# Kernel optimization log

Measured on AMD Instinct MI355X. Metric: run time of the kernel, lower is better.

Reference implementation:

```python
import jax, jax.numpy as jnp
import numpy as np

N = 100000      # nodes
E = 3200000     # edges
G = 256         # graphs in batch
EPS = 1e-5      # BatchNorm eps


def gcn_conv(x, W, b, src, dst, norm):
    # x: [N, Fin] -> [N, Fout]. PyG GCNConv: linear, then sym-normalized
    # scatter-add over edges (self-loops already included in src/dst/norm).
    h = x @ W                                   # [N, Fout]
    msg = h[src] * norm[:, None]                # [E+N, Fout] gather + scale
    out = jax.ops.segment_sum(msg, dst, num_segments=N)
    return out + b


def bn_eval(x, gamma, beta, rm, rv):
    return (x - rm) * jax.lax.rsqrt(rv + EPS) * gamma + beta


def setup_inputs() -> dict:
    key = jax.random.key(0)
    ks = jax.random.split(key, 24)
    x = jax.random.normal(ks[0], (N, 8), dtype=jnp.float32)
    edge_index = jax.random.randint(ks[1], (2, E), 0, N, dtype=jnp.int64)
    batch = jnp.sort(jax.random.randint(ks[2], (N,), 0, G, dtype=jnp.int64))

    def lin(k, fin, fout):
        return jax.random.normal(k, (fin, fout), dtype=jnp.float32) / np.sqrt(fin)

    d = {
        "x": x, "edge_index": edge_index, "batch": batch,
        "W1": lin(ks[3], 8, 64),  "b1": jnp.zeros((64,), jnp.float32),
        "g1": jnp.ones((64,), jnp.float32), "be1": jnp.zeros((64,), jnp.float32),
        "rm1": jax.random.normal(ks[4], (64,), jnp.float32) * 0.1,
        "rv1": jnp.ones((64,), jnp.float32) + jax.random.uniform(ks[5], (64,)) * 0.1,
        "W2": lin(ks[6], 64, 64), "b2": jnp.zeros((64,), jnp.float32),
        "g2": jnp.ones((64,), jnp.float32), "be2": jnp.zeros((64,), jnp.float32),
        "rm2": jax.random.normal(ks[7], (64,), jnp.float32) * 0.1,
        "rv2": jnp.ones((64,), jnp.float32) + jax.random.uniform(ks[8], (64,)) * 0.1,
        "W3": lin(ks[9], 64, 64), "b3": jnp.zeros((64,), jnp.float32),
        "g3": jnp.ones((64,), jnp.float32), "be3": jnp.zeros((64,), jnp.float32),
        "rm3": jax.random.normal(ks[10], (64,), jnp.float32) * 0.1,
        "rv3": jnp.ones((64,), jnp.float32) + jax.random.uniform(ks[11], (64,)) * 0.1,
        "Wr1": lin(ks[12], 64, 64), "br1": jnp.zeros((64,), jnp.float32),
        "Wr2": lin(ks[13], 64, 2),  "br2": jnp.zeros((2,), jnp.float32),
    }
    return d


def reference(x, edge_index, batch,
              W1, b1, g1, be1, rm1, rv1,
              W2, b2, g2, be2, rm2, rv2,
              W3, b3, g3, be3, rm3, rv3,
              Wr1, br1, Wr2, br2):
    # add self-loops once; compute symmetric normalization deg^-1/2
    loops = jnp.arange(N, dtype=edge_index.dtype)
    src = jnp.concatenate([edge_index[0], loops])   # [E+N]
    dst = jnp.concatenate([edge_index[1], loops])
    deg = jax.ops.segment_sum(jnp.ones_like(dst, dtype=x.dtype), dst, num_segments=N)
    dinv = jnp.where(deg > 0, jax.lax.rsqrt(deg), 0.0)
    norm = dinv[src] * dinv[dst]                    # [E+N]

    h = jax.nn.relu(bn_eval(gcn_conv(x, W1, b1, src, dst, norm), g1, be1, rm1, rv1))
    h = jax.nn.relu(bn_eval(gcn_conv(h, W2, b2, src, dst, norm), g2, be2, rm2, rv2))
    h = jax.nn.relu(bn_eval(gcn_conv(h, W3, b3, src, dst, norm), g3, be3, rm3, rv3))

    # global mean pool over graph ids
    sums = jax.ops.segment_sum(h, batch, num_segments=G)           # [G, 64]
    cnts = jax.ops.segment_sum(jnp.ones((N,), h.dtype), batch, num_segments=G)
    pooled = sums / jnp.maximum(cnts, 1.0)[:, None]

    out = jax.nn.relu(pooled @ Wr1 + br1) @ Wr2 + br2              # [G, 2]
    return out
```

## Files before the change

### kernel.cpp

```cpp
#include <hip/hip_runtime.h>

#define NN 100000
#define NE 3200000
#define NG 256
#define NF (NN * 64)
#define FEPS 1e-5f
#define BSH 8
#define NB ((NN + 255) >> 8)
#define CHA 8192

static inline int ceil_div(int a, int b) { return (a + b - 1) / b; }


__global__ __launch_bounds__(256) void kA_hist(const int* __restrict__ dst,
                                               int* __restrict__ bh) {
    __shared__ int lh[NB];
    int t = threadIdx.x;
    for (int b = t; b < NB; b += 256) lh[b] = 0;
    __syncthreads();
    int e0 = blockIdx.x * CHA;
    int e1 = min(e0 + CHA, NE);
    for (int i = e0 + t; i < e1; i += 256) atomicAdd(&lh[dst[i] >> BSH], 1);
    __syncthreads();
    for (int b = t; b < NB; b += 256)
        if (lh[b]) atomicAdd(&bh[b], lh[b]);
}

__global__ __launch_bounds__(512) void kA_scan(const int* __restrict__ bh,
                                               int* __restrict__ bboff,
                                               int* __restrict__ bcur) {
    __shared__ int s[512];
    int t = threadIdx.x;
    int v = (t < NB) ? bh[t] : 0;
    s[t] = v;
    __syncthreads();
    for (int off = 1; off < 512; off <<= 1) {
        int add = (t >= off) ? s[t - off] : 0;
        __syncthreads();
        s[t] += add;
        __syncthreads();
    }
    if (t < NB) {
        int ex = s[t] - v;
        bboff[t] = ex;
        bcur[t] = ex;
    }
    if (t == 0) bboff[NB] = NE;
}

__global__ __launch_bounds__(256) void kA_fill(const int* __restrict__ src,
                                               const int* __restrict__ dst,
                                               int* __restrict__ bcur,
                                               int2* __restrict__ ebuf) {
    __shared__ int lh[NB];
    __shared__ int lbase[NB];
    __shared__ int lcur[NB];
    int t = threadIdx.x;
    for (int b = t; b < NB; b += 256) lh[b] = 0;
    __syncthreads();
    int e0 = blockIdx.x * CHA;
    int e1 = min(e0 + CHA, NE);
    for (int i = e0 + t; i < e1; i += 256) atomicAdd(&lh[dst[i] >> BSH], 1);
    __syncthreads();
    for (int b = t; b < NB; b += 256) {
        int c = lh[b];
        lbase[b] = c ? atomicAdd(&bcur[b], c) : 0;
        lcur[b] = 0;
    }
    __syncthreads();
    for (int i = e0 + t; i < e1; i += 256) {
        int d = dst[i];
        int s = src[i];
        int b = d >> BSH;
        int p = atomicAdd(&lcur[b], 1);
        ebuf[lbase[b] + p] = make_int2(s, d);
    }
}


__global__ __launch_bounds__(256) void kB_hist(const int2* __restrict__ ebuf,
                                               const int* __restrict__ bboff,
                                               int* __restrict__ cnt) {
    __shared__ int lc[256];
    int b = blockIdx.x;
    int t = threadIdx.x;
    lc[t] = 0;
    __syncthreads();
    int st = bboff[b], en = bboff[b + 1];
    for (int i = st + t; i < en; i += 256) atomicAdd(&lc[ebuf[i].y & 255], 1);
    __syncthreads();
    int node = (b << BSH) + t;
    if (node < NN) cnt[node] = lc[t];
}

__global__ __launch_bounds__(256) void k_dinv_xs(const int* __restrict__ cnt,
                                                 const float* __restrict__ x,
                                                 float* __restrict__ dinv,
                                                 float* __restrict__ xs) {
    int i = blockIdx.x * 256 + threadIdx.x;
    if (i >= NN) return;
    float di = rsqrtf((float)cnt[i] + 1.0f);
    dinv[i] = di;
#pragma unroll
    for (int f = 0; f < 8; ++f) xs[i * 8 + f] = x[i * 8 + f] * di;
}

__global__ __launch_bounds__(256) void k_scan1(const int* __restrict__ cnt,
                                               int* __restrict__ bsum) {
    __shared__ int s[256];
    int t = threadIdx.x;
    int i = blockIdx.x * 256 + t;
    s[t] = (i < NN) ? cnt[i] : 0;
    __syncthreads();
    for (int off = 128; off > 0; off >>= 1) {
        if (t < off) s[t] += s[t + off];
        __syncthreads();
    }
    if (t == 0) bsum[blockIdx.x] = s[0];
}

__global__ __launch_bounds__(512) void k_scan2(int* __restrict__ bsum, int nb) {
    __shared__ int s[512];
    int t = threadIdx.x;
    int v = (t < nb) ? bsum[t] : 0;
    s[t] = v;
    __syncthreads();
    for (int off = 1; off < 512; off <<= 1) {
        int add = (t >= off) ? s[t - off] : 0;
        __syncthreads();
        s[t] += add;
        __syncthreads();
    }
    if (t < nb) bsum[t] = s[t] - v;
}

__global__ __launch_bounds__(256) void k_scan3(const int* __restrict__ cnt,
                                               const int* __restrict__ bsum,
                                               int* __restrict__ rowptr) {
    __shared__ int s[256];
    int t = threadIdx.x;
    int i = blockIdx.x * 256 + t;
    int v = (i < NN) ? cnt[i] : 0;
    s[t] = v;
    __syncthreads();
    for (int off = 1; off < 256; off <<= 1) {
        int add = (t >= off) ? s[t - off] : 0;
        __syncthreads();
        s[t] += add;
        __syncthreads();
    }
    if (i < NN) rowptr[i] = s[t] - v + bsum[blockIdx.x];
}

__global__ __launch_bounds__(256) void kB_fill(const int2* __restrict__ ebuf,
                                               const int* __restrict__ bboff,
                                               const int* __restrict__ rowptr,
                                               int* __restrict__ csr) {
    __shared__ int rp[256];
    __shared__ int lc[256];
    int b = blockIdx.x;
    int t = threadIdx.x;
    int node = (b << BSH) + t;
    rp[t] = (node < NN) ? rowptr[node] : 0;
    lc[t] = 0;
    __syncthreads();
    int st = bboff[b], en = bboff[b + 1];
    for (int i = st + t; i < en; i += 256) {
        int2 e = ebuf[i];
        int dl = e.y & 255;
        int p = atomicAdd(&lc[dl], 1);
        csr[rp[dl] + p] = e.x;
    }
}


__global__ __launch_bounds__(256) void k_gxf8(const float* __restrict__ xs,
                                              const int* __restrict__ rowptr,
                                              const int* __restrict__ cnt,
                                              const float* __restrict__ dinv,
                                              const int* __restrict__ csr,
                                              const float* __restrict__ W,
                                              const float* __restrict__ b,
                                              const float* __restrict__ g,
                                              const float* __restrict__ be,
                                              const float* __restrict__ rm,
                                              const float* __restrict__ rv,
                                              float* __restrict__ out) {
    __shared__ float Ws[512];
    int tid = threadIdx.x;
    for (int i = tid; i < 512; i += 256) Ws[i] = W[i];
    __syncthreads();
    int wave = (blockIdx.x * 256 + tid) >> 6;
    int lane = tid & 63;
    if (wave >= NN) return;
    int es = lane >> 3, f = lane & 7;
    int st = rowptr[wave], n = cnt[wave];
    float acc = 0.f;
    for (int k0 = 0; k0 < n; k0 += 8) {
        int kk = k0 + es;
        if (kk < n) acc += xs[csr[st + kk] * 8 + f];
    }
    acc += __shfl_xor(acc, 8, 64);
    acc += __shfl_xor(acc, 16, 64);
    acc += __shfl_xor(acc, 32, 64);
    float di = dinv[wave];
    float pf = (acc + xs[wave * 8 + f]) * di;
    float scale = g[lane] * rsqrtf(rv[lane] + FEPS);
    float shift = be[lane] + (b[lane] - rm[lane]) * scale;
    float o = 0.f;
#pragma unroll
    for (int k = 0; k < 8; ++k)
        o = fmaf(__shfl(pf, k, 64), Ws[k * 64 + lane], o);
    o = fmaxf(fmaf(o, scale, shift), 0.f);
    out[wave * 64 + lane] = o * di;
}

template <bool SCALE_OUT>
__global__ __launch_bounds__(256) void k_gxf64(const float* __restrict__ Hin,
                                               const int* __restrict__ rowptr,
                                               const int* __restrict__ cnt,
                                               const float* __restrict__ dinv,
                                               const int* __restrict__ csr,
                                               const float* __restrict__ W,
                                               const float* __restrict__ b,
                                               const float* __restrict__ g,
                                               const float* __restrict__ be,
                                               const float* __restrict__ rm,
                                               const float* __restrict__ rv,
                                               float* __restrict__ out) {
    __shared__ float Ws[4096];
    int tid = threadIdx.x;
    for (int i = tid; i < 4096; i += 256) Ws[i] = W[i];
    __syncthreads();
    int wave = (blockIdx.x * 256 + tid) >> 6;
    int lane = tid & 63;
    if (wave >= NN) return;
    int st = rowptr[wave], n = cnt[wave];
    float acc = Hin[wave * 64 + lane];
    int k = 0;
    for (; k + 4 <= n; k += 4) {
        int s0 = csr[st + k];
        int s1 = csr[st + k + 1];
        int s2 = csr[st + k + 2];
        int s3 = csr[st + k + 3];
        float v0 = Hin[s0 * 64 + lane];
        float v1 = Hin[s1 * 64 + lane];
        float v2 = Hin[s2 * 64 + lane];
        float v3 = Hin[s3 * 64 + lane];
        acc += v0; acc += v1; acc += v2; acc += v3;
    }
    for (; k < n; ++k) acc += Hin[csr[st + k] * 64 + lane];
    float di = dinv[wave];
    float pf = acc * di;
    float scale = g[lane] * rsqrtf(rv[lane] + FEPS);
    float shift = be[lane] + (b[lane] - rm[lane]) * scale;
    float o = 0.f;
#pragma unroll
    for (int k2 = 0; k2 < 64; ++k2)
        o = fmaf(__shfl(pf, k2, 64), Ws[k2 * 64 + lane], o);
    o = fmaxf(fmaf(o, scale, shift), 0.f);
    if (SCALE_OUT) o *= di;
    out[wave * 64 + lane] = o;
}


__global__ __launch_bounds__(256) void k_pool(const float* __restrict__ h,
                                              const int* __restrict__ batch,
                                              float* __restrict__ sums,
                                              float* __restrict__ cnts) {
    const int CHUNK = 32;
    int gw = (blockIdx.x * 256 + threadIdx.x) >> 6;
    int lane = threadIdx.x & 63;
    int nw = (gridDim.x * 256) >> 6;
    int nchunks = (NN + CHUNK - 1) / CHUNK;
    for (int c = gw; c < nchunks; c += nw) {
        int n0 = c * CHUNK;
        int n1 = min(n0 + CHUNK, NN);
        int gcur = batch[n0];
        float accf = 0.f;
        float cntf = 0.f;
        for (int n = n0; n < n1; ++n) {
            int gg = batch[n];
            if (gg != gcur) {
                atomicAdd(&sums[gcur * 64 + lane], accf);
                if (lane == 0) atomicAdd(&cnts[gcur], cntf);
                accf = 0.f;
                cntf = 0.f;
                gcur = gg;
            }
            accf += h[n * 64 + lane];
            cntf += 1.f;
        }
        atomicAdd(&sums[gcur * 64 + lane], accf);
        if (lane == 0) atomicAdd(&cnts[gcur], cntf);
    }
}

__global__ __launch_bounds__(256) void k_head(const float* __restrict__ sums,
                                              const float* __restrict__ cnts,
                                              const float* __restrict__ Wr1,
                                              const float* __restrict__ br1,
                                              const float* __restrict__ Wr2,
                                              const float* __restrict__ br2,
                                              float* __restrict__ out) {
    int wave = (blockIdx.x * 256 + threadIdx.x) >> 6;
    int lane = threadIdx.x & 63;
    if (wave >= NG) return;
    float c = fmaxf(cnts[wave], 1.0f);
    float pooled = sums[wave * 64 + lane] / c;
    float acc = 0.f;
#pragma unroll
    for (int k = 0; k < 64; ++k)
        acc = fmaf(__shfl(pooled, k, 64), Wr1[k * 64 + lane], acc);
    float hid = fmaxf(acc + br1[lane], 0.f);
    float o0 = hid * Wr2[lane * 2 + 0];
    float o1 = hid * Wr2[lane * 2 + 1];
#pragma unroll
    for (int off = 32; off > 0; off >>= 1) {
        o0 += __shfl_xor(o0, off, 64);
        o1 += __shfl_xor(o1, off, 64);
    }
    if (lane == 0) {
        out[wave * 2 + 0] = o0 + br2[0];
        out[wave * 2 + 1] = o1 + br2[1];
    }
}

extern "C" void kernel_launch(void* const* d_in, const int* in_sizes, int n_in,
                              void* d_out, int out_size, void* d_ws, size_t ws_size,
                              hipStream_t stream) {
    const float* x   = (const float*)d_in[0];
    const int*   ei  = (const int*)d_in[1];
    const int*   bat = (const int*)d_in[2];
    const float* W1  = (const float*)d_in[3];
    const float* b1  = (const float*)d_in[4];
    const float* g1  = (const float*)d_in[5];
    const float* be1 = (const float*)d_in[6];
    const float* rm1 = (const float*)d_in[7];
    const float* rv1 = (const float*)d_in[8];
    const float* W2  = (const float*)d_in[9];
    const float* b2  = (const float*)d_in[10];
    const float* g2  = (const float*)d_in[11];
    const float* be2 = (const float*)d_in[12];
    const float* rm2 = (const float*)d_in[13];
    const float* rv2 = (const float*)d_in[14];
    const float* W3  = (const float*)d_in[15];
    const float* b3  = (const float*)d_in[16];
    const float* g3  = (const float*)d_in[17];
    const float* be3 = (const float*)d_in[18];
    const float* rm3 = (const float*)d_in[19];
    const float* rv3 = (const float*)d_in[20];
    const float* Wr1 = (const float*)d_in[21];
    const float* br1 = (const float*)d_in[22];
    const float* Wr2 = (const float*)d_in[23];
    const float* br2 = (const float*)d_in[24];
    float* out = (float*)d_out;

    int*   cnt    = (int*)d_ws;
    int*   rowptr = cnt + NN;
    int*   bsum   = rowptr + NN;
    int*   bh     = bsum + 512;
    int*   bboff  = bh + NB;
    int*   bcur   = bboff + NB + 1;
    float* dinv   = (float*)(bcur + NB);
    int*   csr    = (int*)(dinv + NN);
    float* xs     = (float*)(csr + NE);
    float* A      = xs + NN * 8;
    float* B      = A + NF;
    float* sums   = B + NF;
    float* cnts   = sums + NG * 64;
    int2*  ebuf   = (int2*)A;

    const int* srcI = ei;
    const int* dstI = ei + NE;

    const int gA = ceil_div(NE, CHA);
    const int gN = ceil_div(NN, 256);
    const int gW = ceil_div(NN * 64, 256);

    hipMemsetAsync(bh, 0, NB * sizeof(int), stream);
    hipMemsetAsync(sums, 0, (NG * 64 + NG) * sizeof(float), stream);

    kA_hist<<<gA, 256, 0, stream>>>(dstI, bh);
    kA_scan<<<1, 512, 0, stream>>>(bh, bboff, bcur);
    kA_fill<<<gA, 256, 0, stream>>>(srcI, dstI, bcur, ebuf);

    kB_hist<<<NB, 256, 0, stream>>>(ebuf, bboff, cnt);
    k_dinv_xs<<<gN, 256, 0, stream>>>(cnt, x, dinv, xs);
    k_scan1<<<gN, 256, 0, stream>>>(cnt, bsum);
    k_scan2<<<1, 512, 0, stream>>>(bsum, gN);
    k_scan3<<<gN, 256, 0, stream>>>(cnt, bsum, rowptr);
    kB_fill<<<NB, 256, 0, stream>>>(ebuf, bboff, rowptr, csr);

    k_gxf8<<<gW, 256, 0, stream>>>(xs, rowptr, cnt, dinv, csr,
                                   W1, b1, g1, be1, rm1, rv1, A);
    k_gxf64<true><<<gW, 256, 0, stream>>>(A, rowptr, cnt, dinv, csr,
                                          W2, b2, g2, be2, rm2, rv2, B);
    k_gxf64<false><<<gW, 256, 0, stream>>>(B, rowptr, cnt, dinv, csr,
                                           W3, b3, g3, be3, rm3, rv3, A);

    k_pool<<<800, 256, 0, stream>>>(A, bat, sums, cnts);
    k_head<<<ceil_div(NG * 64, 256), 256, 0, stream>>>(sums, cnts, Wr1, br1, Wr2, br2, out);
}
```

Before: 701.9 us.

## Store node activations in fp16 and batch CSR index loads via wave shuffles

Intermediate node feature buffers (xs, A, B) are now stored as half precision while accumulation and the dense transforms stay in fp32. This halves the bytes moved by the random neighbour gathers, which dominate the GCN aggregation kernels. The 64-wide aggregation kernel also loads up to 64 CSR neighbour indices per wave in one coalesced read, broadcasts them with shuffles, and unrolls the gather by 8 into two accumulators. The weight matvec uses four partial sums for more instruction-level parallelism. The cost is reduced activation precision and narrower 2-byte per-lane loads, and the workspace is relaid so the edge staging buffer aliases the two half buffers exactly.

New measurement: 648.6 us. 7.6% less time.

```diff
diff --git a/kernel.cpp b/kernel.cpp
--- a/kernel.cpp
+++ b/kernel.cpp
@@ -1,4 +1,5 @@
 #include <hip/hip_runtime.h>
+#include <hip/hip_fp16.h>
 
 #define NN 100000
 #define NE 3200000
@@ -96,13 +97,13 @@
 __global__ __launch_bounds__(256) void k_dinv_xs(const int* __restrict__ cnt,
                                                  const float* __restrict__ x,
                                                  float* __restrict__ dinv,
-                                                 float* __restrict__ xs) {
+                                                 __half* __restrict__ xs) {
     int i = blockIdx.x * 256 + threadIdx.x;
     if (i >= NN) return;
     float di = rsqrtf((float)cnt[i] + 1.0f);
     dinv[i] = di;
 #pragma unroll
-    for (int f = 0; f < 8; ++f) xs[i * 8 + f] = x[i * 8 + f] * di;
+    for (int f = 0; f < 8; ++f) xs[i * 8 + f] = __float2half(x[i * 8 + f] * di);
 }
 
 __global__ __launch_bounds__(256) void k_scan1(const int* __restrict__ cnt,
@@ -174,7 +175,7 @@
 }
 
 
-__global__ __launch_bounds__(256) void k_gxf8(const float* __restrict__ xs,
+__global__ __launch_bounds__(256) void k_gxf8(const __half* __restrict__ xs,
                                               const int* __restrict__ rowptr,
                                               const int* __restrict__ cnt,
                                               const float* __restrict__ dinv,
@@ -185,7 +186,7 @@
                                               const float* __restrict__ be,
                                               const float* __restrict__ rm,
                                               const float* __restrict__ rv,
-                                              float* __restrict__ out) {
+                                              __half* __restrict__ out) {
     __shared__ float Ws[512];
     int tid = threadIdx.x;
     for (int i = tid; i < 512; i += 256) Ws[i] = W[i];
@@ -198,13 +199,13 @@
     float acc = 0.f;
     for (int k0 = 0; k0 < n; k0 += 8) {
         int kk = k0 + es;
-        if (kk < n) acc += xs[csr[st + kk] * 8 + f];
+        if (kk < n) acc += __half2float(xs[csr[st + kk] * 8 + f]);
     }
     acc += __shfl_xor(acc, 8, 64);
     acc += __shfl_xor(acc, 16, 64);
     acc += __shfl_xor(acc, 32, 64);
     float di = dinv[wave];
-    float pf = (acc + xs[wave * 8 + f]) * di;
+    float pf = (acc + __half2float(xs[wave * 8 + f])) * di;
     float scale = g[lane] * rsqrtf(rv[lane] + FEPS);
     float shift = be[lane] + (b[lane] - rm[lane]) * scale;
     float o = 0.f;
@@ -212,11 +213,11 @@
     for (int k = 0; k < 8; ++k)
         o = fmaf(__shfl(pf, k, 64), Ws[k * 64 + lane], o);
     o = fmaxf(fmaf(o, scale, shift), 0.f);
-    out[wave * 64 + lane] = o * di;
+    out[wave * 64 + lane] = __float2half(o * di);
 }
 
 template <bool SCALE_OUT>
-__global__ __launch_bounds__(256) void k_gxf64(const float* __restrict__ Hin,
+__global__ __launch_bounds__(256) void k_gxf64(const __half* __restrict__ Hin,
                                                const int* __restrict__ rowptr,
                                                const int* __restrict__ cnt,
                                                const float* __restrict__ dinv,
@@ -227,7 +228,7 @@
                                                const float* __restrict__ be,
                                                const float* __restrict__ rm,
                                                const float* __restrict__ rv,
-                                               float* __restrict__ out) {
+                                               __half* __restrict__ out) {
     __shared__ float Ws[4096];
     int tid = threadIdx.x;
     for (int i = tid; i < 4096; i += 256) Ws[i] = W[i];
@@ -236,35 +237,60 @@
     int lane = tid & 63;
     if (wave >= NN) return;
     int st = rowptr[wave], n = cnt[wave];
-    float acc = Hin[wave * 64 + lane];
+    float a0 = __half2float(Hin[wave * 64 + lane]);
+    float a1 = 0.f;
     int k = 0;
-    for (; k + 4 <= n; k += 4) {
-        int s0 = csr[st + k];
-        int s1 = csr[st + k + 1];
-        int s2 = csr[st + k + 2];
-        int s3 = csr[st + k + 3];
-        float v0 = Hin[s0 * 64 + lane];
-        float v1 = Hin[s1 * 64 + lane];
-        float v2 = Hin[s2 * 64 + lane];
-        float v3 = Hin[s3 * 64 + lane];
-        acc += v0; acc += v1; acc += v2; acc += v3;
-    }
-    for (; k < n; ++k) acc += Hin[csr[st + k] * 64 + lane];
+    while (k < n) {
+        int rem = n - k;
+        int chunk = rem < 64 ? rem : 64;
+        int eidx = (lane < chunk) ? csr[st + k + lane] : 0;
+        int j = 0;
+        for (; j + 8 <= chunk; j += 8) {
+            int s0 = __shfl(eidx, j + 0, 64);
+            int s1 = __shfl(eidx, j + 1, 64);
+            int s2 = __shfl(eidx, j + 2, 64);
+            int s3 = __shfl(eidx, j + 3, 64);
+            int s4 = __shfl(eidx, j + 4, 64);
+            int s5 = __shfl(eidx, j + 5, 64);
+            int s6 = __shfl(eidx, j + 6, 64);
+            int s7 = __shfl(eidx, j + 7, 64);
+            float v0 = __half2float(Hin[s0 * 64 + lane]);
+            float v1 = __half2float(Hin[s1 * 64 + lane]);
+            float v2 = __half2float(Hin[s2 * 64 + lane]);
+            float v3 = __half2float(Hin[s3 * 64 + lane]);
+            float v4 = __half2float(Hin[s4 * 64 + lane]);
+            float v5 = __half2float(Hin[s5 * 64 + lane]);
+            float v6 = __half2float(Hin[s6 * 64 + lane]);
+            float v7 = __half2float(Hin[s7 * 64 + lane]);
+            a0 += (v0 + v1) + (v2 + v3);
+            a1 += (v4 + v5) + (v6 + v7);
+        }
+        for (; j < chunk; ++j) {
+            int s = __shfl(eidx, j, 64);
+            a0 += __half2float(Hin[s * 64 + lane]);
+        }
+        k += chunk;
+    }
     float di = dinv[wave];
-    float pf = acc * di;
+    float pf = (a0 + a1) * di;
     float scale = g[lane] * rsqrtf(rv[lane] + FEPS);
     float shift = be[lane] + (b[lane] - rm[lane]) * scale;
-    float o = 0.f;
+    float o0 = 0.f, o1 = 0.f, o2 = 0.f, o3 = 0.f;
 #pragma unroll
-    for (int k2 = 0; k2 < 64; ++k2)
-        o = fmaf(__shfl(pf, k2, 64), Ws[k2 * 64 + lane], o);
+    for (int k2 = 0; k2 < 64; k2 += 4) {
+        o0 = fmaf(__shfl(pf, k2 + 0, 64), Ws[(k2 + 0) * 64 + lane], o0);
+        o1 = fmaf(__shfl(pf, k2 + 1, 64), Ws[(k2 + 1) * 64 + lane], o1);
+        o2 = fmaf(__shfl(pf, k2 + 2, 64), Ws[(k2 + 2) * 64 + lane], o2);
+        o3 = fmaf(__shfl(pf, k2 + 3, 64), Ws[(k2 + 3) * 64 + lane], o3);
+    }
+    float o = (o0 + o1) + (o2 + o3);
     o = fmaxf(fmaf(o, scale, shift), 0.f);
     if (SCALE_OUT) o *= di;
-    out[wave * 64 + lane] = o;
-}
-
-
-__global__ __launch_bounds__(256) void k_pool(const float* __restrict__ h,
+    out[wave * 64 + lane] = __float2half(o);
+}
+
+
+__global__ __launch_bounds__(256) void k_pool(const __half* __restrict__ h,
                                               const int* __restrict__ batch,
                                               float* __restrict__ sums,
                                               float* __restrict__ cnts) {
@@ -288,7 +314,7 @@
                 cntf = 0.f;
                 gcur = gg;
             }
-            accf += h[n * 64 + lane];
+            accf += __half2float(h[n * 64 + lane]);
             cntf += 1.f;
         }
         atomicAdd(&sums[gcur * 64 + lane], accf);
@@ -356,20 +382,20 @@
     const float* br2 = (const float*)d_in[24];
     float* out = (float*)d_out;
 
-    int*   cnt    = (int*)d_ws;
-    int*   rowptr = cnt + NN;
-    int*   bsum   = rowptr + NN;
-    int*   bh     = bsum + 512;
-    int*   bboff  = bh + NB;
-    int*   bcur   = bboff + NB + 1;
-    float* dinv   = (float*)(bcur + NB);
-    int*   csr    = (int*)(dinv + NN);
-    float* xs     = (float*)(csr + NE);
-    float* A      = xs + NN * 8;
-    float* B      = A + NF;
-    float* sums   = B + NF;
-    float* cnts   = sums + NG * 64;
-    int2*  ebuf   = (int2*)A;
+    int*    cnt    = (int*)d_ws;
+    int*    rowptr = cnt + NN;
+    int*    bsum   = rowptr + NN;
+    int*    bh     = bsum + 512;
+    int*    bboff  = bh + NB;
+    int*    bcur   = bboff + NB + 1;
+    float*  dinv   = (float*)(bcur + NB);
+    int*    csr    = (int*)(dinv + NN);
+    __half* xs     = (__half*)(csr + NE);
+    float*  sums   = (float*)(xs + NN * 8);
+    float*  cnts   = sums + NG * 64;
+    __half* A      = (__half*)(cnts + NG);
+    __half* B      = A + NF;
+    int2*   ebuf   = (int2*)A;
 
     const int* srcI = ei;
     const int* dstI = ei + NE;
```
